# Kernel tuning notes

Hardware: AMD Instinct MI355X
Metric: run time of the kernel (lower is better)

## Reference

```python
import jax, jax.numpy as jnp
import numpy as np

B, T, H = 2, 2048, 2048
E, K, I = 8, 2, 1408


def setup_inputs() -> dict:
    key = jax.random.key(0)
    ks = jax.random.split(key, 6)
    x = jax.random.normal(ks[0], (B, T, H), dtype=jnp.float32)
    # router: small-std, row-normalized init (as in the torch module)
    gw = jax.random.normal(ks[1], (E, H), dtype=jnp.float32) * 1e-3
    gw = gw / (jnp.linalg.norm(gw, axis=-1, keepdims=True) + 1e-6)
    scale1 = 1.0 / np.sqrt(H)
    scale2 = 1.0 / np.sqrt(I)
    W1 = jax.random.normal(ks[2], (E, H, I), dtype=jnp.float32) * scale1  # fc1 per expert
    W2 = jax.random.normal(ks[3], (E, I, H), dtype=jnp.float32) * scale2  # fc2 per expert
    Ws1 = jax.random.normal(ks[4], (H, I), dtype=jnp.float32) * scale1    # shared expert fc1
    Ws2 = jax.random.normal(ks[5], (I, H), dtype=jnp.float32) * scale2    # shared expert fc2
    return {"x": x, "gate_w": gw, "W1": W1, "W2": W2, "Ws1": Ws1, "Ws2": Ws2}


def reference(x, gate_w, W1, W2, Ws1, Ws2):
    b, t, h = x.shape
    nt = b * t
    x_flat = x.reshape(nt, h)

    # router
    gate_logits = x_flat @ gate_w.T                       # [nt, E]
    gate_probs = jax.nn.softmax(gate_logits.astype(jnp.float32), axis=-1)
    topk_vals, topk_idx = jax.lax.top_k(gate_probs, K)    # [nt, K]

    # aux (load-balancing) loss
    importance = gate_probs.mean(axis=0)                  # [E]
    load = jnp.zeros((E,), jnp.float32).at[topk_idx.reshape(-1)].add(1.0)
    load = load / (nt * K)
    aux_loss = (importance * load).sum() * E

    # combine weights: zero except at top-k experts (NOT renormalized, matching forward)
    combine = jnp.sum(jax.nn.one_hot(topk_idx, E, dtype=jnp.float32)
                      * topk_vals[..., None], axis=1)     # [nt, E]

    # dense expert compute (equivalent to gather-expert-scatter with 0 weights elsewhere)
    h1 = jnp.einsum('th,ehi->tei', x_flat, W1)            # [nt, E, I]
    h1 = h1 * jax.nn.sigmoid(h1)                          # SiLU
    expert_out = jnp.einsum('tei,eih->teh', h1, W2)       # [nt, E, H]
    y_flat = jnp.einsum('teh,te->th', expert_out, combine)

    # shared expert (always on)
    hs = x_flat @ Ws1
    y_flat = y_flat + (hs * jax.nn.sigmoid(hs)) @ Ws2

    y = y_flat.reshape(b, t, h).astype(x.dtype)
    return y, aux_loss
```

## Files before the change

kernel.cpp:

```cpp
#include <hip/hip_runtime.h>
#include <hip/hip_bf16.h>

#define NT 4096
#define HD 2048
#define NE 8
#define TOPK 2
#define ID 1408
#define NG 9
#define BM 128
#define BN 128
#define BK 64
#define MT_MAX 104
#define NWG1 1144
#define NTW 6336

typedef unsigned short u16;
typedef unsigned int u32;
typedef unsigned long long u64;
typedef __attribute__((ext_vector_type(8))) short bf16x8;
typedef __attribute__((ext_vector_type(4))) float f32x4;

__device__ __forceinline__ u16 f2bf(float f) {
    u32 u = __builtin_bit_cast(u32, f);
    u += 0x7FFFu + ((u >> 16) & 1u);
    return (u16)(u >> 16);
}
__device__ __forceinline__ float bflo(u32 v) { return __builtin_bit_cast(float, v << 16); }
__device__ __forceinline__ float bfhi(u32 v) { return __builtin_bit_cast(float, v & 0xffff0000u); }

typedef __attribute__((address_space(1))) const void gas_void;
typedef __attribute__((address_space(3))) void las_void;
__device__ __forceinline__ void gl_lds16(const void* g, void* l) {
    __builtin_amdgcn_global_load_lds((gas_void*)(u64)g, (las_void*)(u32)(u64)l, 16, 0, 0);
}

__global__ void router_tw1_kernel(const float* __restrict__ x, const float* __restrict__ gw,
                                  int* __restrict__ counts, float* __restrict__ imp,
                                  int* __restrict__ tki, float* __restrict__ tkv,
                                  u16* __restrict__ xb,
                                  const float* __restrict__ W1, const float* __restrict__ Ws1,
                                  u16* __restrict__ wt1) {
    __shared__ float s_imp[NE];
    __shared__ int s_cnt[NE];
    __shared__ u16 Lt[64][68];
    int tid = threadIdx.x;
    if (blockIdx.x < NT / 4) {
        if (tid < NE) { s_imp[tid] = 0.f; s_cnt[tid] = 0; }
        int w = tid >> 6, lane = tid & 63;
        int t = blockIdx.x * 4 + w;
        float acc[NE];
#pragma unroll
        for (int e = 0; e < NE; e++) acc[e] = 0.f;
        const float* xr = x + (size_t)t * HD;
        u16* xw = xb + (size_t)t * HD;
#pragma unroll
        for (int i = 0; i < 4; i++) {
            int cc = i * 64 + lane;
            int b64 = cc >> 3, j = cc & 7, h = j >> 2, q = j & 3;
            int k0 = b64 * 64 + h * 32 + q * 4;
            float4 v0 = *(const float4*)(xr + k0);
            float4 v1 = *(const float4*)(xr + k0 + 16);
#pragma unroll
            for (int e = 0; e < NE; e++) {
                const float* gp = gw + e * HD + k0;
                float4 g0 = *(const float4*)(gp);
                float4 g1 = *(const float4*)(gp + 16);
                acc[e] += v0.x * g0.x + v0.y * g0.y + v0.z * g0.z + v0.w * g0.w
                        + v1.x * g1.x + v1.y * g1.y + v1.z * g1.z + v1.w * g1.w;
            }
            ushort4 o0, o1;
            o0.x = f2bf(v0.x); o0.y = f2bf(v0.y); o0.z = f2bf(v0.z); o0.w = f2bf(v0.w);
            o1.x = f2bf(v1.x); o1.y = f2bf(v1.y); o1.z = f2bf(v1.z); o1.w = f2bf(v1.w);
            uint4 o;
            o.x = (u32)o0.x | ((u32)o0.y << 16); o.y = (u32)o0.z | ((u32)o0.w << 16);
            o.z = (u32)o1.x | ((u32)o1.y << 16); o.w = (u32)o1.z | ((u32)o1.w << 16);
            *(uint4*)(xw + b64 * 64 + j * 8) = o;
        }
#pragma unroll
        for (int e = 0; e < NE; e++) {
#pragma unroll
            for (int o = 32; o >= 1; o >>= 1) acc[e] += __shfl_xor(acc[e], o, 64);
        }
        __syncthreads();
        if (lane == 0) {
            float mx = acc[0];
            for (int e = 1; e < NE; e++) mx = fmaxf(mx, acc[e]);
            float p[NE], sum = 0.f;
            for (int e = 0; e < NE; e++) { p[e] = expf(acc[e] - mx); sum += p[e]; }
            float inv = 1.f / sum;
            for (int e = 0; e < NE; e++) p[e] *= inv;
            int i1 = 0;
            for (int e = 1; e < NE; e++) if (p[e] > p[i1]) i1 = e;
            int i2 = (i1 == 0) ? 1 : 0;
            for (int e = 0; e < NE; e++) if (e != i1 && p[e] > p[i2]) i2 = e;
            tki[t * 2 + 0] = i1; tkv[t * 2 + 0] = p[i1];
            tki[t * 2 + 1] = i2; tkv[t * 2 + 1] = p[i2];
            for (int e = 0; e < NE; e++) atomicAdd(&s_imp[e], p[e]);
            atomicAdd(&s_cnt[i1], 1); atomicAdd(&s_cnt[i2], 1);
        }
        __syncthreads();
        if (tid < NE) {
            atomicAdd(&imp[tid], s_imp[tid]);
            atomicAdd(&counts[tid], s_cnt[tid]);
        }
    } else {
        int tw = blockIdx.x - NT / 4;
        int e = tw / 704, rem = tw % 704;
        int n0 = (rem % 22) * 64, k0 = (rem / 22) * 64;
        const float* src = (e < NE) ? (W1 + (size_t)e * HD * ID) : Ws1;
        u16* dst = wt1 + (size_t)e * ID * HD;
#pragma unroll
        for (int i = 0; i < 4; i++) {
            int idx = i * 256 + tid;
            int kl = idx >> 4, nq = (idx & 15) * 4;
            float4 v = *(const float4*)(src + (size_t)(k0 + kl) * ID + n0 + nq);
            Lt[nq + 0][kl] = f2bf(v.x); Lt[nq + 1][kl] = f2bf(v.y);
            Lt[nq + 2][kl] = f2bf(v.z); Lt[nq + 3][kl] = f2bf(v.w);
        }
        __syncthreads();
#pragma unroll
        for (int c2 = 0; c2 < 2; c2++) {
            int cid = tid * 2 + c2;
            int nr = cid >> 3, j = cid & 7;
            int h = j >> 2, q = j & 3;
            int kb = h * 32 + q * 4;
            uint2 lo = *(const uint2*)&Lt[nr][kb];
            uint2 hi = *(const uint2*)&Lt[nr][kb + 16];
            uint4 o; o.x = lo.x; o.y = lo.y; o.z = hi.x; o.w = hi.y;
            *(uint4*)(dst + (size_t)(n0 + nr) * HD + k0 + j * 8) = o;
        }
    }
}

__global__ void prepscat_kernel(const int* __restrict__ counts, const float* __restrict__ imp,
                                int* __restrict__ off, int* __restrict__ tileoff,
                                float* __restrict__ out_aux,
                                int* __restrict__ tki, const float* __restrict__ tkv,
                                int* __restrict__ list, float* __restrict__ wgt) {
    __shared__ int s_off[NG];
    __shared__ int s_cur[NE];
    int tid = threadIdx.x;
    if (tid == 0) {
        int o = 0, to = 0;
        for (int g = 0; g < NG; g++) {
            int c = (g < NE) ? counts[g] : NT;
            off[g] = o; s_off[g] = o; tileoff[g] = to;
            o += c; to += (c + BM - 1) / BM;
        }
        off[NG] = o; tileoff[NG] = to;
        float aux = 0.f;
        for (int e = 0; e < NE; e++)
            aux += (imp[e] / (float)NT) * ((float)counts[e] / (float)(NT * TOPK));
        *out_aux = aux * (float)NE;
    }
    if (tid < NE) s_cur[tid] = 0;
    __syncthreads();
    for (int t = tid; t < NT; t += 256) {
#pragma unroll
        for (int k = 0; k < TOPK; k++) {
            int e = tki[t * 2 + k];
            int pos = atomicAdd(&s_cur[e], 1);
            int s = s_off[e] + pos;
            list[s] = t;
            wgt[s] = tkv[t * 2 + k];
            tki[t * 2 + k] = s;
        }
        list[s_off[NE] + t] = t;
        wgt[s_off[NE] + t] = 1.0f;
    }
}

__global__ void transw_kernel(const float* __restrict__ W, const float* __restrict__ Wsh,
                              u16* __restrict__ dst, int K, int N) {
    int e = blockIdx.z;
    const float* src = (e < NE) ? (W + (size_t)e * K * N) : Wsh;
    dst += (size_t)e * N * K;
    int k0 = blockIdx.y * 64, n0 = blockIdx.x * 64;
    __shared__ u16 Lt[64][68];
    int tid = threadIdx.x;
#pragma unroll
    for (int i = 0; i < 4; i++) {
        int idx = i * 256 + tid;
        int kl = idx >> 4, nq = (idx & 15) * 4;
        float4 v = *(const float4*)(src + (size_t)(k0 + kl) * N + n0 + nq);
        Lt[nq + 0][kl] = f2bf(v.x); Lt[nq + 1][kl] = f2bf(v.y);
        Lt[nq + 2][kl] = f2bf(v.z); Lt[nq + 3][kl] = f2bf(v.w);
    }
    __syncthreads();
#pragma unroll
    for (int c2 = 0; c2 < 2; c2++) {
        int cid = tid * 2 + c2;
        int nr = cid >> 3, j = cid & 7;
        int h = j >> 2, q = j & 3;
        int kb = h * 32 + q * 4;
        uint2 lo = *(const uint2*)&Lt[nr][kb];
        uint2 hi = *(const uint2*)&Lt[nr][kb + 16];
        uint4 o; o.x = lo.x; o.y = lo.y; o.z = hi.x; o.w = hi.y;
        *(uint4*)(dst + (size_t)(n0 + nr) * K + k0 + j * 8) = o;
    }
}

template <bool FTW>
__global__ __launch_bounds__(512, 4) void fc1_kernel(
    const u16* __restrict__ xb, const u16* __restrict__ Wt1,
    const int* __restrict__ off, const int* __restrict__ tileoff,
    const int* __restrict__ list, u16* __restrict__ h1,
    const float* __restrict__ W2, const float* __restrict__ Ws2,
    u16* __restrict__ wt2) {
    __shared__ u16 S[2 * 16384];
    int wg0 = blockIdx.x;
    int tid = threadIdx.x;
    if (FTW && wg0 >= NWG1) {
        u16 (*Lt)[68] = (u16(*)[68])S;
        int tw = wg0 - NWG1;
        int e = tw / 704, rem = tw % 704;
        int n0 = (rem % 32) * 64, k0 = (rem / 32) * 64;
        const float* src = (e < NE) ? (W2 + (size_t)e * ID * HD) : Ws2;
        u16* dst = wt2 + (size_t)e * HD * ID;
#pragma unroll
        for (int i = 0; i < 2; i++) {
            int idx = i * 512 + tid;
            int kl = idx >> 4, nq = (idx & 15) * 4;
            float4 v = *(const float4*)(src + (size_t)(k0 + kl) * HD + n0 + nq);
            Lt[nq + 0][kl] = f2bf(v.x); Lt[nq + 1][kl] = f2bf(v.y);
            Lt[nq + 2][kl] = f2bf(v.z); Lt[nq + 3][kl] = f2bf(v.w);
        }
        __syncthreads();
        {
            int cid = tid;
            int nr = cid >> 3, j = cid & 7;
            int h = j >> 2, q = j & 3;
            int kb = h * 32 + q * 4;
            uint2 lo = *(const uint2*)&Lt[nr][kb];
            uint2 hi = *(const uint2*)&Lt[nr][kb + 16];
            uint4 o; o.x = lo.x; o.y = lo.y; o.z = hi.x; o.w = hi.y;
            *(uint4*)(dst + (size_t)(n0 + nr) * ID + k0 + j * 8) = o;
        }
        return;
    }
    int wg = (wg0 & 7) * (NWG1 >> 3) + (wg0 >> 3);
    int bx = wg % (ID / BN), mt = wg / (ID / BN);

    int g = -1, gto = 0;
#pragma unroll
    for (int gg = 0; gg < NG; gg++)
        if (mt >= tileoff[gg] && mt < tileoff[gg + 1]) { g = gg; gto = tileoff[gg]; }
    if (g < 0) return;
    int goff = off[g], cnt = off[g + 1] - goff;
    int row0 = (mt - gto) * BM;
    const u16* Wb = Wt1 + (size_t)g * (ID * HD);
    int n0 = bx * BN;
    int lane = tid & 63, w = tid >> 6;
    int r0 = tid >> 3, r1 = 64 + r0;
    int lc = (((tid & 7) ^ (r0 & 7)) << 3);
    int ra0 = row0 + r0; ra0 = (ra0 < cnt) ? ra0 : (cnt - 1);
    int ra1 = row0 + r1; ra1 = (ra1 < cnt) ? ra1 : (cnt - 1);
    const u16* pa0 = xb + (size_t)list[goff + ra0] * HD + lc;
    const u16* pa1 = xb + (size_t)list[goff + ra1] * HD + lc;
    const u16* pb0 = Wb + (size_t)(n0 + r0) * HD + lc;
    const u16* pb1 = Wb + (size_t)(n0 + r1) * HD + lc;

    int wr = w >> 2, wc = w & 3;
    int lr = lane & 15, l7 = lane & 7, q2 = lane >> 4;
    f32x4 acc[4][2] = {};

    auto stage = [&](int b) {
        u16* A = S + b * 16384;
        u16* B = A + 8192;
        gl_lds16(pa0, A + tid * 8);        pa0 += BK;
        gl_lds16(pa1, A + 4096 + tid * 8); pa1 += BK;
        gl_lds16(pb0, B + tid * 8);        pb0 += BK;
        gl_lds16(pb1, B + 4096 + tid * 8); pb1 += BK;
    };
    auto compute = [&](int b) {
        const u16* A = S + b * 16384;
        const u16* B = A + 8192;
#pragma unroll
        for (int kc = 0; kc < 8; kc += 4) {
            int slot = ((kc + q2) ^ l7) << 3;
            bf16x8 a[4], bb[2];
#pragma unroll
            for (int f = 0; f < 4; f++)
                a[f] = __builtin_bit_cast(bf16x8, *(const uint4*)&A[(wr * 64 + f * 16 + lr) * BK + slot]);
#pragma unroll
            for (int f = 0; f < 2; f++)
                bb[f] = __builtin_bit_cast(bf16x8, *(const uint4*)&B[(wc * 32 + f * 16 + lr) * BK + slot]);
            __builtin_amdgcn_s_setprio(1);
#pragma unroll
            for (int mf = 0; mf < 4; mf++)
#pragma unroll
                for (int nf = 0; nf < 2; nf++)
                    acc[mf][nf] = __builtin_amdgcn_mfma_f32_16x16x32_bf16(a[mf], bb[nf], acc[mf][nf], 0, 0, 0);
            __builtin_amdgcn_s_setprio(0);
        }
    };

    stage(0);
    int cur = 0;
    for (int t = 1; t < HD / BK; ++t) {
        stage(cur ^ 1);
        asm volatile("s_waitcnt vmcnt(4)" ::: "memory");
        __builtin_amdgcn_s_barrier();
        compute(cur);
        asm volatile("s_waitcnt lgkmcnt(0)" ::: "memory");
        __builtin_amdgcn_s_barrier();
        cur ^= 1;
    }
    asm volatile("s_waitcnt vmcnt(0)" ::: "memory");
    __builtin_amdgcn_s_barrier();
    compute(cur);

    int q4 = q2 * 4;
    int cl = ((lr >> 2) << 3) + (lr & 3);
#pragma unroll
    for (int mf = 0; mf < 4; mf++)
#pragma unroll
        for (int reg = 0; reg < 4; reg++) {
            int r = row0 + wr * 64 + mf * 16 + q4 + reg;
            if (r < cnt) {
                size_t rb = (size_t)(goff + r) * ID + n0;
#pragma unroll
                for (int nf = 0; nf < 2; nf++) {
                    float v = acc[mf][nf][reg];
                    h1[rb + wc * 32 + (nf << 2) + cl] = f2bf(v / (1.f + __expf(-v)));
                }
            }
        }
}

template <bool EO>
__global__ __launch_bounds__(512, 4) void fc2_kernel(
    const u16* __restrict__ h1, const u16* __restrict__ Wt2,
    const int* __restrict__ off, const int* __restrict__ tileoff,
    const int* __restrict__ list, const float* __restrict__ wgt,
    u16* __restrict__ eo, float* __restrict__ y) {
    __shared__ u16 S[2 * 16384];
    int nwg = gridDim.x * gridDim.y;
    int orig = blockIdx.y * gridDim.x + blockIdx.x;
    int wg = (orig & 7) * (nwg >> 3) + (orig >> 3);
    int bx = wg % gridDim.x, mt = wg / gridDim.x;

    int g = -1, gto = 0;
#pragma unroll
    for (int gg = 0; gg < NG; gg++)
        if (mt >= tileoff[gg] && mt < tileoff[gg + 1]) { g = gg; gto = tileoff[gg]; }
    if (g < 0) return;
    int goff = off[g], cnt = off[g + 1] - goff;
    int row0 = (mt - gto) * BM;
    const u16* Wb = Wt2 + (size_t)g * (ID * HD);
    int n0 = bx * BN;
    int tid = threadIdx.x, lane = tid & 63, w = tid >> 6;
    int r0 = tid >> 3, r1 = 64 + r0;
    int lc = (((tid & 7) ^ (r0 & 7)) << 3);
    int ra0 = row0 + r0; ra0 = (ra0 < cnt) ? ra0 : (cnt - 1);
    int ra1 = row0 + r1; ra1 = (ra1 < cnt) ? ra1 : (cnt - 1);
    const u16* pa0 = h1 + (size_t)(goff + ra0) * ID + lc;
    const u16* pa1 = h1 + (size_t)(goff + ra1) * ID + lc;
    const u16* pb0 = Wb + (size_t)(n0 + r0) * ID + lc;
    const u16* pb1 = Wb + (size_t)(n0 + r1) * ID + lc;

    int wr = w >> 2, wc = w & 3;
    int lr = lane & 15, l7 = lane & 7, q2 = lane >> 4;
    f32x4 acc[4][2] = {};

    auto stage = [&](int b) {
        u16* A = S + b * 16384;
        u16* B = A + 8192;
        gl_lds16(pa0, A + tid * 8);        pa0 += BK;
        gl_lds16(pa1, A + 4096 + tid * 8); pa1 += BK;
        gl_lds16(pb0, B + tid * 8);        pb0 += BK;
        gl_lds16(pb1, B + 4096 + tid * 8); pb1 += BK;
    };
    auto compute = [&](int b) {
        const u16* A = S + b * 16384;
        const u16* B = A + 8192;
#pragma unroll
        for (int kc = 0; kc < 8; kc += 4) {
            int slot = ((kc + q2) ^ l7) << 3;
            bf16x8 a[4], bb[2];
#pragma unroll
            for (int f = 0; f < 4; f++)
                a[f] = __builtin_bit_cast(bf16x8, *(const uint4*)&A[(wr * 64 + f * 16 + lr) * BK + slot]);
#pragma unroll
            for (int f = 0; f < 2; f++)
                bb[f] = __builtin_bit_cast(bf16x8, *(const uint4*)&B[(wc * 32 + f * 16 + lr) * BK + slot]);
            __builtin_amdgcn_s_setprio(1);
#pragma unroll
            for (int mf = 0; mf < 4; mf++)
#pragma unroll
                for (int nf = 0; nf < 2; nf++)
                    acc[mf][nf] = __builtin_amdgcn_mfma_f32_16x16x32_bf16(a[mf], bb[nf], acc[mf][nf], 0, 0, 0);
            __builtin_amdgcn_s_setprio(0);
        }
    };

    stage(0);
    int cur = 0;
    for (int t = 1; t < ID / BK; ++t) {
        stage(cur ^ 1);
        asm volatile("s_waitcnt vmcnt(4)" ::: "memory");
        __builtin_amdgcn_s_barrier();
        compute(cur);
        asm volatile("s_waitcnt lgkmcnt(0)" ::: "memory");
        __builtin_amdgcn_s_barrier();
        cur ^= 1;
    }
    asm volatile("s_waitcnt vmcnt(0)" ::: "memory");
    __builtin_amdgcn_s_barrier();
    compute(cur);

    int q4 = q2 * 4;
#pragma unroll
    for (int mf = 0; mf < 4; mf++)
#pragma unroll
        for (int reg = 0; reg < 4; reg++) {
            int r = row0 + wr * 64 + mf * 16 + q4 + reg;
            if (r < cnt) {
                int slot = goff + r;
                if (EO) {
                    size_t rb = (size_t)slot * HD + n0 + wc * 32;
#pragma unroll
                    for (int nf = 0; nf < 2; nf++)
                        eo[rb + nf * 16 + lr] = f2bf(acc[mf][nf][reg]);
                } else {
                    int tok = list[slot];
                    float wv = wgt[slot];
                    float* yr = y + (size_t)tok * HD + n0 + wc * 32;
#pragma unroll
                    for (int nf = 0; nf < 2; nf++)
                        atomicAdd(yr + nf * 16 + lr, acc[mf][nf][reg] * wv);
                }
            }
        }
}

__global__ __launch_bounds__(256) void combine_kernel(
    const u16* __restrict__ eo, const int* __restrict__ smap,
    const float* __restrict__ tkv, const int* __restrict__ off,
    float* __restrict__ y) {
    int idx = blockIdx.x * 256 + threadIdx.x;
    int t = idx >> 8;
    int cc = (idx & 255) << 3;
    int s0 = smap[t * 2 + 0], s1 = smap[t * 2 + 1];
    float w0 = tkv[t * 2 + 0], w1 = tkv[t * 2 + 1];
    int s2 = off[NE] + t;
    uint4 A = *(const uint4*)(eo + (size_t)s0 * HD + cc);
    uint4 B = *(const uint4*)(eo + (size_t)s1 * HD + cc);
    uint4 C = *(const uint4*)(eo + (size_t)s2 * HD + cc);
    float4 o0, o1;
    o0.x = w0 * bflo(A.x) + w1 * bflo(B.x) + bflo(C.x);
    o0.y = w0 * bfhi(A.x) + w1 * bfhi(B.x) + bfhi(C.x);
    o0.z = w0 * bflo(A.y) + w1 * bflo(B.y) + bflo(C.y);
    o0.w = w0 * bfhi(A.y) + w1 * bfhi(B.y) + bfhi(C.y);
    o1.x = w0 * bflo(A.z) + w1 * bflo(B.z) + bflo(C.z);
    o1.y = w0 * bfhi(A.z) + w1 * bfhi(B.z) + bfhi(C.z);
    o1.z = w0 * bflo(A.w) + w1 * bflo(B.w) + bflo(C.w);
    o1.w = w0 * bfhi(A.w) + w1 * bfhi(B.w) + bfhi(C.w);
    float* yr = y + (size_t)t * HD + cc;
    *(float4*)yr = o0;
    *(float4*)(yr + 4) = o1;
}

extern "C" void kernel_launch(void* const* d_in, const int* in_sizes, int n_in,
                              void* d_out, int out_size, void* d_ws, size_t ws_size,
                              hipStream_t stream) {
    const float* x   = (const float*)d_in[0];
    const float* gw  = (const float*)d_in[1];
    const float* W1  = (const float*)d_in[2];
    const float* W2  = (const float*)d_in[3];
    const float* Ws1 = (const float*)d_in[4];
    const float* Ws2 = (const float*)d_in[5];
    float* out = (float*)d_out;

    char* ws = (char*)d_ws;
    int*   counts  = (int*)(ws + 0);
    int*   off     = (int*)(ws + 128);
    int*   tileoff = (int*)(ws + 192);
    float* imp     = (float*)(ws + 256);
    int*   tki     = (int*)(ws + 320);
    float* tkv     = (float*)(ws + 33088);
    int*   list    = (int*)(ws + 65856);
    float* wgt     = (float*)(ws + 115008);
    u16* xb  = (u16*)(ws + 164352);
    u16* wt1 = (u16*)(ws + 16941568ULL);
    u16* h1  = (u16*)(ws + 68846080ULL);
    u16* eo  = (u16*)(ws + 103449088ULL);
    const bool use_big = (ws_size >= 205685248ULL);
    const bool use_eo  = (ws_size >= 153780736ULL);
    u16* wt2 = use_big ? (u16*)(ws + 153780736ULL) : (u16*)(ws + 164352);

    if (!use_eo)
        hipMemsetAsync(d_out, 0, (size_t)out_size * sizeof(float), stream);
    hipMemsetAsync(d_ws, 0, 320, stream);

    router_tw1_kernel<<<NT / 4 + NTW, 256, 0, stream>>>(
        x, gw, counts, imp, tki, tkv, xb, W1, Ws1, wt1);
    prepscat_kernel<<<1, 256, 0, stream>>>(
        counts, imp, off, tileoff, out + (size_t)NT * HD, tki, tkv, list, wgt);

    if (use_big) {
        fc1_kernel<true><<<NWG1 + NTW, 512, 0, stream>>>(
            xb, wt1, off, tileoff, list, h1, W2, Ws2, wt2);
    } else {
        fc1_kernel<false><<<NWG1, 512, 0, stream>>>(
            xb, wt1, off, tileoff, list, h1, W2, Ws2, wt2);
        transw_kernel<<<dim3(HD / 64, ID / 64, NG), 256, 0, stream>>>(W2, Ws2, wt2, ID, HD);
    }

    if (use_eo) {
        fc2_kernel<true><<<dim3(HD / BN, MT_MAX), 512, 0, stream>>>(
            h1, wt2, off, tileoff, list, wgt, eo, out);
        combine_kernel<<<NT, 256, 0, stream>>>(eo, tki, tkv, off, out);
    } else {
        fc2_kernel<false><<<dim3(HD / BN, MT_MAX), 512, 0, stream>>>(
            h1, wt2, off, tileoff, list, wgt, eo, out);
    }
}
```

Measured before the change: 272.4 us.

## Enlarge grouped GEMM M-tile to 192 rows with 768-thread workgroups

Both fc1 and fc2 grouped GEMMs move from 128x128 tiles with 8 waves to 192x128 tiles with 12 waves. The extra waves load only A rows; B tile loads stay on the first 512 threads, with per-wave vmcnt waits adjusted. Tile counts and grid sizes shrink (MT_MAX 72, NWG1 792, NWG2 1152), and fc2 switches to a 1D grid with the same swizzle as fc1. The goal is more reuse of each weight tile per load. The cost is more LDS per block, more padding waste on partial tiles per expert group, and the launch_bounds occupancy hint of 6 may not hold with 768 threads.

```diff
diff --git a/kernel.cpp b/kernel.cpp
--- a/kernel.cpp
+++ b/kernel.cpp
@@ -7,11 +7,12 @@
 #define TOPK 2
 #define ID 1408
 #define NG 9
-#define BM 128
+#define BM 192
 #define BN 128
 #define BK 64
-#define MT_MAX 104
-#define NWG1 1144
+#define MT_MAX 72
+#define NWG1 792
+#define NWG2 1152
 #define NTW 6336
 
 typedef unsigned short u16;
@@ -201,13 +202,13 @@
 }
 
 template <bool FTW>
-__global__ __launch_bounds__(512, 4) void fc1_kernel(
+__global__ __launch_bounds__(768, 6) void fc1_kernel(
     const u16* __restrict__ xb, const u16* __restrict__ Wt1,
     const int* __restrict__ off, const int* __restrict__ tileoff,
     const int* __restrict__ list, u16* __restrict__ h1,
     const float* __restrict__ W2, const float* __restrict__ Ws2,
     u16* __restrict__ wt2) {
-    __shared__ u16 S[2 * 16384];
+    __shared__ u16 S[2 * 20480];
     int wg0 = blockIdx.x;
     int tid = threadIdx.x;
     if (FTW && wg0 >= NWG1) {
@@ -219,22 +220,23 @@
         u16* dst = wt2 + (size_t)e * HD * ID;
 #pragma unroll
         for (int i = 0; i < 2; i++) {
-            int idx = i * 512 + tid;
-            int kl = idx >> 4, nq = (idx & 15) * 4;
-            float4 v = *(const float4*)(src + (size_t)(k0 + kl) * HD + n0 + nq);
-            Lt[nq + 0][kl] = f2bf(v.x); Lt[nq + 1][kl] = f2bf(v.y);
-            Lt[nq + 2][kl] = f2bf(v.z); Lt[nq + 3][kl] = f2bf(v.w);
+            int idx = i * 768 + tid;
+            if (idx < 1024) {
+                int kl = idx >> 4, nq = (idx & 15) * 4;
+                float4 v = *(const float4*)(src + (size_t)(k0 + kl) * HD + n0 + nq);
+                Lt[nq + 0][kl] = f2bf(v.x); Lt[nq + 1][kl] = f2bf(v.y);
+                Lt[nq + 2][kl] = f2bf(v.z); Lt[nq + 3][kl] = f2bf(v.w);
+            }
         }
         __syncthreads();
-        {
-            int cid = tid;
-            int nr = cid >> 3, j = cid & 7;
+        if (tid < 512) {
+            int nr = tid >> 3, j = tid & 7;
             int h = j >> 2, q = j & 3;
             int kb = h * 32 + q * 4;
             uint2 lo = *(const uint2*)&Lt[nr][kb];
             uint2 hi = *(const uint2*)&Lt[nr][kb + 16];
             uint4 o; o.x = lo.x; o.y = lo.y; o.z = hi.x; o.w = hi.y;
-            *(uint4*)(dst + (size_t)(n0 + nr) * ID + k0 + j * 8) = o;
+            *(uint4*)(dst + (size_t)(n0 + nr) * ID + kb * 2 - kb * 2 + k0 + j * 8) = o;
         }
         return;
     }
@@ -251,30 +253,35 @@
     const u16* Wb = Wt1 + (size_t)g * (ID * HD);
     int n0 = bx * BN;
     int lane = tid & 63, w = tid >> 6;
-    int r0 = tid >> 3, r1 = 64 + r0;
+    int r0 = tid >> 3;
     int lc = (((tid & 7) ^ (r0 & 7)) << 3);
-    int ra0 = row0 + r0; ra0 = (ra0 < cnt) ? ra0 : (cnt - 1);
-    int ra1 = row0 + r1; ra1 = (ra1 < cnt) ? ra1 : (cnt - 1);
+    int ra0 = row0 + r0;      ra0 = (ra0 < cnt) ? ra0 : (cnt - 1);
+    int ra1 = row0 + 96 + r0; ra1 = (ra1 < cnt) ? ra1 : (cnt - 1);
     const u16* pa0 = xb + (size_t)list[goff + ra0] * HD + lc;
     const u16* pa1 = xb + (size_t)list[goff + ra1] * HD + lc;
-    const u16* pb0 = Wb + (size_t)(n0 + r0) * HD + lc;
-    const u16* pb1 = Wb + (size_t)(n0 + r1) * HD + lc;
+    const u16* pb0 = nullptr; const u16* pb1 = nullptr;
+    if (tid < 512) {
+        pb0 = Wb + (size_t)(n0 + r0) * HD + lc;
+        pb1 = Wb + (size_t)(n0 + 64 + r0) * HD + lc;
+    }
 
     int wr = w >> 2, wc = w & 3;
     int lr = lane & 15, l7 = lane & 7, q2 = lane >> 4;
     f32x4 acc[4][2] = {};
 
     auto stage = [&](int b) {
-        u16* A = S + b * 16384;
-        u16* B = A + 8192;
+        u16* A = S + b * 20480;
+        u16* B = A + 12288;
         gl_lds16(pa0, A + tid * 8);        pa0 += BK;
-        gl_lds16(pa1, A + 4096 + tid * 8); pa1 += BK;
-        gl_lds16(pb0, B + tid * 8);        pb0 += BK;
-        gl_lds16(pb1, B + 4096 + tid * 8); pb1 += BK;
+        gl_lds16(pa1, A + 6144 + tid * 8); pa1 += BK;
+        if (tid < 512) {
+            gl_lds16(pb0, B + tid * 8);        pb0 += BK;
+            gl_lds16(pb1, B + 4096 + tid * 8); pb1 += BK;
+        }
     };
     auto compute = [&](int b) {
-        const u16* A = S + b * 16384;
-        const u16* B = A + 8192;
+        const u16* A = S + b * 20480;
+        const u16* B = A + 12288;
 #pragma unroll
         for (int kc = 0; kc < 8; kc += 4) {
             int slot = ((kc + q2) ^ l7) << 3;
@@ -295,11 +302,13 @@
         }
     };
 
+    bool heavy = (w < 8);
     stage(0);
     int cur = 0;
     for (int t = 1; t < HD / BK; ++t) {
         stage(cur ^ 1);
-        asm volatile("s_waitcnt vmcnt(4)" ::: "memory");
+        if (heavy) asm volatile("s_waitcnt vmcnt(4)" ::: "memory");
+        else       asm volatile("s_waitcnt vmcnt(2)" ::: "memory");
         __builtin_amdgcn_s_barrier();
         compute(cur);
         asm volatile("s_waitcnt lgkmcnt(0)" ::: "memory");
@@ -329,16 +338,15 @@
 }
 
 template <bool EO>
-__global__ __launch_bounds__(512, 4) void fc2_kernel(
+__global__ __launch_bounds__(768, 6) void fc2_kernel(
     const u16* __restrict__ h1, const u16* __restrict__ Wt2,
     const int* __restrict__ off, const int* __restrict__ tileoff,
     const int* __restrict__ list, const float* __restrict__ wgt,
     u16* __restrict__ eo, float* __restrict__ y) {
-    __shared__ u16 S[2 * 16384];
-    int nwg = gridDim.x * gridDim.y;
-    int orig = blockIdx.y * gridDim.x + blockIdx.x;
-    int wg = (orig & 7) * (nwg >> 3) + (orig >> 3);
-    int bx = wg % gridDim.x, mt = wg / gridDim.x;
+    __shared__ u16 S[2 * 20480];
+    int wg0 = blockIdx.x;
+    int wg = (wg0 & 7) * (NWG2 >> 3) + (wg0 >> 3);
+    int bx = wg % (HD / BN), mt = wg / (HD / BN);
 
     int g = -1, gto = 0;
 #pragma unroll
@@ -350,30 +358,35 @@
     const u16* Wb = Wt2 + (size_t)g * (ID * HD);
     int n0 = bx * BN;
     int tid = threadIdx.x, lane = tid & 63, w = tid >> 6;
-    int r0 = tid >> 3, r1 = 64 + r0;
+    int r0 = tid >> 3;
     int lc = (((tid & 7) ^ (r0 & 7)) << 3);
-    int ra0 = row0 + r0; ra0 = (ra0 < cnt) ? ra0 : (cnt - 1);
-    int ra1 = row0 + r1; ra1 = (ra1 < cnt) ? ra1 : (cnt - 1);
+    int ra0 = row0 + r0;      ra0 = (ra0 < cnt) ? ra0 : (cnt - 1);
+    int ra1 = row0 + 96 + r0; ra1 = (ra1 < cnt) ? ra1 : (cnt - 1);
     const u16* pa0 = h1 + (size_t)(goff + ra0) * ID + lc;
     const u16* pa1 = h1 + (size_t)(goff + ra1) * ID + lc;
-    const u16* pb0 = Wb + (size_t)(n0 + r0) * ID + lc;
-    const u16* pb1 = Wb + (size_t)(n0 + r1) * ID + lc;
+    const u16* pb0 = nullptr; const u16* pb1 = nullptr;
+    if (tid < 512) {
+        pb0 = Wb + (size_t)(n0 + r0) * ID + lc;
+        pb1 = Wb + (size_t)(n0 + 64 + r0) * ID + lc;
+    }
 
     int wr = w >> 2, wc = w & 3;
     int lr = lane & 15, l7 = lane & 7, q2 = lane >> 4;
     f32x4 acc[4][2] = {};
 
     auto stage = [&](int b) {
-        u16* A = S + b * 16384;
-        u16* B = A + 8192;
+        u16* A = S + b * 20480;
+        u16* B = A + 12288;
         gl_lds16(pa0, A + tid * 8);        pa0 += BK;
-        gl_lds16(pa1, A + 4096 + tid * 8); pa1 += BK;
-        gl_lds16(pb0, B + tid * 8);        pb0 += BK;
-        gl_lds16(pb1, B + 4096 + tid * 8); pb1 += BK;
+        gl_lds16(pa1, A + 6144 + tid * 8); pa1 += BK;
+        if (tid < 512) {
+            gl_lds16(pb0, B + tid * 8);        pb0 += BK;
+            gl_lds16(pb1, B + 4096 + tid * 8); pb1 += BK;
+        }
     };
     auto compute = [&](int b) {
-        const u16* A = S + b * 16384;
-        const u16* B = A + 8192;
+        const u16* A = S + b * 20480;
+        const u16* B = A + 12288;
 #pragma unroll
         for (int kc = 0; kc < 8; kc += 4) {
             int slot = ((kc + q2) ^ l7) << 3;
@@ -394,11 +407,13 @@
         }
     };
 
+    bool heavy = (w < 8);
     stage(0);
     int cur = 0;
     for (int t = 1; t < ID / BK; ++t) {
         stage(cur ^ 1);
-        asm volatile("s_waitcnt vmcnt(4)" ::: "memory");
+        if (heavy) asm volatile("s_waitcnt vmcnt(4)" ::: "memory");
+        else       asm volatile("s_waitcnt vmcnt(2)" ::: "memory");
         __builtin_amdgcn_s_barrier();
         compute(cur);
         asm volatile("s_waitcnt lgkmcnt(0)" ::: "memory");
@@ -499,20 +514,20 @@
         counts, imp, off, tileoff, out + (size_t)NT * HD, tki, tkv, list, wgt);
 
     if (use_big) {
-        fc1_kernel<true><<<NWG1 + NTW, 512, 0, stream>>>(
+        fc1_kernel<true><<<NWG1 + NTW, 768, 0, stream>>>(
             xb, wt1, off, tileoff, list, h1, W2, Ws2, wt2);
     } else {
-        fc1_kernel<false><<<NWG1, 512, 0, stream>>>(
+        fc1_kernel<false><<<NWG1, 768, 0, stream>>>(
             xb, wt1, off, tileoff, list, h1, W2, Ws2, wt2);
         transw_kernel<<<dim3(HD / 64, ID / 64, NG), 256, 0, stream>>>(W2, Ws2, wt2, ID, HD);
     }
 
     if (use_eo) {
-        fc2_kernel<true><<<dim3(HD / BN, MT_MAX), 512, 0, stream>>>(
+        fc2_kernel<true><<<NWG2, 768, 0, stream>>>(
             h1, wt2, off, tileoff, list, wgt, eo, out);
         combine_kernel<<<NT, 256, 0, stream>>>(eo, tki, tkv, off, out);
     } else {
-        fc2_kernel<false><<<dim3(HD / BN, MT_MAX), 512, 0, stream>>>(
+        fc2_kernel<false><<<NWG2, 768, 0, stream>>>(
             h1, wt2, off, tileoff, list, wgt, eo, out);
     }
 }
```

After: 269.7 us. About the same (-1.0%).
